# Optimization experiments

Measured on AMD Instinct MI355X. Metric: run time of the kernel, lower is better.

## Reference

```python
import math
import jax, jax.numpy as jnp
import numpy as np

B, H, W, C = 2, 32, 32, 64
K = 15
G = 4
GC = C // G
K2 = K * K
RED = C // 4
MAX_SIGMA = 0.5


def setup_inputs() -> dict:
    key = jax.random.key(0)
    ks = jax.random.split(key, 32)
    f32 = jnp.float32

    def rn(k, shape, std):
        return (jax.random.normal(k, shape) * std).astype(f32)

    lin = 1.0 / math.sqrt(C)
    inp = {
        'x': jax.random.normal(ks[0], (B, H, W, C), f32),
        'raw_sigma': jnp.asarray(math.log(math.exp(0.3) - 1.0), f32),
        'base_offset_scale': jnp.asarray(0.1, f32),
        # input/output projections (stored [in,out])
        'w_ip': rn(ks[1], (C, C), lin), 'b_ip': jnp.zeros((C,), f32),
        'w_op': rn(ks[2], (C, C), lin), 'b_op': jnp.zeros((C,), f32),
        # dw_conv: depthwise 3x3 (HWIO, I=1) then pointwise 1x1 ([in,out])
        'w_dw': rn(ks[3], (3, 3, 1, C), 1.0 / 3.0), 'b_dw': jnp.zeros((C,), f32),
        'w_pw': rn(ks[4], (C, C), lin), 'b_pw': jnp.zeros((C,), f32),
        # offset / mask heads (original zero-inits; small random to exercise path)
        'w_off': rn(ks[5], (C, G * K2 * 2), 0.01), 'b_off': rn(ks[6], (G * K2 * 2,), 0.01),
        'w_msk': rn(ks[7], (C, G * K2), 0.01), 'b_msk': rn(ks[8], (G * K2,), 0.01),
        # kernel MLP: 2 -> 32 -> 32 -> G*GC
        'w_k1': rn(ks[9], (2, 32), 0.5), 'b_k1': jnp.zeros((32,), f32),
        'w_k2': rn(ks[10], (32, 32), 1.0 / math.sqrt(32)), 'b_k2': jnp.zeros((32,), f32),
        'w_k3': rn(ks[11], (32, G * GC), 1.0 / math.sqrt(32)), 'b_k3': jnp.zeros((G * GC,), f32),
        # SE block
        'w_fc1': rn(ks[12], (C, RED), lin), 'b_fc1': jnp.zeros((RED,), f32),
        'w_fc2': rn(ks[13], (RED, C), 1.0 / math.sqrt(RED)), 'b_fc2': jnp.zeros((C,), f32),
    }
    return inp


def _forward(x, raw_sigma, base_offset_scale, w_ip, b_ip, w_op, b_op, w_dw, b_dw,
             w_pw, b_pw, w_off, b_off, w_msk, b_msk, w_k1, b_k1, w_k2, b_k2,
             w_k3, b_k3, w_fc1, b_fc1, w_fc2, b_fc2):
    Bx, Hx, Wx, Cx = x.shape
    sigma = jnp.clip(jax.nn.softplus(raw_sigma), 1e-3, MAX_SIGMA)
    grid = jnp.linspace(-0.5, 0.5, K)  # [K]

    x_proj = x @ w_ip + b_ip  # [B,H,W,C]

    # depthwise 3x3 (SAME) + SiLU + pointwise 1x1
    y = jax.lax.conv_general_dilated(
        x, w_dw, (1, 1), 'SAME',
        dimension_numbers=('NHWC', 'HWIO', 'NHWC'), feature_group_count=Cx) + b_dw
    x_dw = jax.nn.silu(y) @ w_pw + b_pw  # [B,H,W,C]

    # Gaussian envelope over kernel grid, normalized
    env = jnp.exp(-(grid[:, None] ** 2 + grid[None, :] ** 2) / (2.0 * sigma ** 2))
    env = env / jnp.maximum(env.sum(), 1e-8)
    env_flat = env.reshape(1, 1, 1, 1, K2)

    gh, gw = jnp.meshgrid(grid, grid, indexing='ij')
    pos = jnp.stack([gh.ravel(), gw.ravel()], axis=-1) * 2.0  # [K2,2]
    hkw = jax.nn.silu(pos @ w_k1 + b_k1)
    hkw = jax.nn.silu(hkw @ w_k2 + b_k2)
    kw_raw = hkw @ w_k3 + b_k3  # [K2, G*GC]
    # faithful to torch view quirk: (K,K,G,gc) memory reinterpreted as (G,K2,gc)
    kw = kw_raw.reshape(G, K2, GC).reshape(1, 1, 1, G, K2, GC)

    offsets = (x_dw @ w_off + b_off).reshape(Bx, Hx, Wx, G, K2, 2) * base_offset_scale
    raw_mask = (x_dw @ w_msk + b_msk).reshape(Bx, Hx, Wx, G, K2) * env_flat
    attn = jnp.nan_to_num(jax.nn.softmax(raw_mask, axis=-1))

    # absolute sampling locations
    ref = jnp.linspace(-(K // 2), K // 2, K)
    rh, rw = jnp.meshgrid(ref, ref, indexing='ij')  # [K,K]
    pos_h = jnp.arange(Hx, dtype=x.dtype).reshape(1, Hx, 1, 1, 1)
    pos_w = jnp.arange(Wx, dtype=x.dtype).reshape(1, 1, Wx, 1, 1)
    abs_h = pos_h + rh.ravel().reshape(1, 1, 1, 1, K2) + offsets[..., 0]
    abs_w = pos_w + rw.ravel().reshape(1, 1, 1, 1, K2) + offsets[..., 1]
    ah = jnp.clip(abs_h, 0.0, Hx - 1)
    aw = jnp.clip(abs_w, 0.0, Wx - 1)
    h_f = jnp.clip(jnp.floor(ah).astype(jnp.int32), 0, Hx - 1)
    w_f = jnp.clip(jnp.floor(aw).astype(jnp.int32), 0, Wx - 1)
    h_c = jnp.minimum(h_f + 1, Hx - 1)
    w_c = jnp.minimum(w_f + 1, Wx - 1)
    hw = ah - h_f.astype(x.dtype)
    ww = aw - w_f.astype(x.dtype)
    valid = (~((abs_h < 0) | (abs_h > Hx - 1) | (abs_w < 0) | (abs_w > Wx - 1))).astype(x.dtype)

    xg = x_proj.reshape(Bx, Hx, Wx, G, GC)
    b_idx = jnp.arange(Bx).reshape(Bx, 1, 1, 1, 1)
    g_idx = jnp.arange(G).reshape(1, 1, 1, G, 1)
    v_ff = xg[b_idx, h_f, w_f, g_idx]  # [B,H,W,G,K2,GC]
    v_fc = xg[b_idx, h_f, w_c, g_idx]
    v_cf = xg[b_idx, h_c, w_f, g_idx]
    v_cc = xg[b_idx, h_c, w_c, g_idx]
    sampled = (v_ff * ((1 - hw) * (1 - ww) * valid)[..., None]
               + v_fc * ((1 - hw) * ww * valid)[..., None]
               + v_cf * (hw * (1 - ww) * valid)[..., None]
               + v_cc * (hw * ww * valid)[..., None])
    sampled = sampled * kw
    output = (sampled * attn[..., None]).sum(axis=4).reshape(Bx, Hx, Wx, Cx)

    # SE block (no mask, no bias)
    pooled = output.mean(axis=(1, 2), keepdims=True)
    se = jax.nn.silu(pooled @ w_fc1 + b_fc1) @ w_fc2 + b_fc2
    output = output * jax.nn.sigmoid(se)

    out = output @ w_op + b_op
    offset_reg = (offsets ** 2).mean()
    entropy = -(attn * jnp.log(attn + 1e-8)).sum(axis=-1).mean()
    return out, offset_reg, -entropy


def reference(x, raw_sigma, base_offset_scale, w_ip, b_ip, w_op, b_op, w_dw, b_dw,
              w_pw, b_pw, w_off, b_off, w_msk, b_msk, w_k1, b_k1, w_k2, b_k2,
              w_k3, b_k3, w_fc1, b_fc1, w_fc2, b_fc2):
    return _forward(x, raw_sigma, base_offset_scale, w_ip, b_ip, w_op, b_op,
                    w_dw, b_dw, w_pw, b_pw, w_off, b_off, w_msk, b_msk,
                    w_k1, b_k1, w_k2, b_k2, w_k3, b_k3, w_fc1, b_fc1, w_fc2, b_fc2)
```

## Files before the change

### kernel.cpp

```cpp
#include <hip/hip_runtime.h>
#include <math.h>

#define KK2 225
#define NPIX 2048
#define OFFC 1800
#define MSKC 900

#define WS_KW    0
#define WS_XPROJ 16384
#define WS_XDW   (16384+131072)
#define WS_OUT   (16384+2*131072)
#define WS_POOL  (16384+3*131072)
#define WS_GATE  (WS_POOL+128)
#define WS_ENTP  (WS_GATE+128)
#define WS_OFFP  (WS_ENTP+2048)
#define WS_PART2 (WS_OFFP+512)

__device__ __forceinline__ float silu(float a) { return a / (1.f + __expf(-a)); }

__global__ __launch_bounds__(256) void k_pre(
    const float* __restrict__ x,
    const float* __restrict__ w_ip, const float* __restrict__ b_ip,
    const float* __restrict__ w_dw, const float* __restrict__ b_dw,
    const float* __restrict__ w_pw, const float* __restrict__ b_pw,
    const float* __restrict__ w_k1, const float* __restrict__ b_k1,
    const float* __restrict__ w_k2, const float* __restrict__ b_k2,
    const float* __restrict__ w_k3, const float* __restrict__ b_k3,
    float* __restrict__ ws)
{
  int t = threadIdx.x;
  if (blockIdx.x < 512) {
    int px = t >> 6, c = t & 63;
    int pix = blockIdx.x * 4 + px;
    int b = pix >> 10, h = (pix >> 5) & 31, w = pix & 31;
    __shared__ float xs[4][64], ys[4][64];
    xs[px][c] = x[pix*64 + c];
    float acc = b_dw[c];
    #pragma unroll
    for (int dh = -1; dh <= 1; dh++) {
      int hh = h + dh;
      if (hh < 0 || hh > 31) continue;
      #pragma unroll
      for (int dw2 = -1; dw2 <= 1; dw2++) {
        int wp = w + dw2;
        if (wp < 0 || wp > 31) continue;
        acc += x[(((b*32 + hh)*32 + wp) << 6) + c] * w_dw[((dh+1)*3 + (dw2+1))*64 + c];
      }
    }
    ys[px][c] = silu(acc);
    __syncthreads();
    float p1 = b_ip[c], p2 = b_pw[c];
    #pragma unroll 8
    for (int k = 0; k < 64; k++) {
      p1 += xs[px][k] * w_ip[k*64 + c];
      p2 += ys[px][k] * w_pw[k*64 + c];
    }
    ws[WS_XPROJ + pix*64 + c] = p1;
    ws[WS_XDW   + pix*64 + c] = p2;
  } else {
    __shared__ float h1s[4][32], h2s[4][32];
    int tl = t >> 6, lane = t & 63;
    int tap = (blockIdx.x - 512) * 4 + tl;
    int tapc = min(tap, KK2 - 1);
    int i = tapc / 15, j = tapc % 15;
    float gi = -0.5f + (float)i * (1.0f/14.0f);
    float gj = -0.5f + (float)j * (1.0f/14.0f);
    float p0 = gi * 2.f, p1 = gj * 2.f;
    if (lane < 32) {
      float a = p0 * w_k1[lane] + p1 * w_k1[32 + lane] + b_k1[lane];
      h1s[tl][lane] = silu(a);
    }
    __syncthreads();
    if (lane < 32) {
      float a = b_k2[lane];
      #pragma unroll
      for (int q = 0; q < 32; q++) a += h1s[tl][q] * w_k2[q*32 + lane];
      h2s[tl][lane] = silu(a);
    }
    __syncthreads();
    float a = b_k3[lane];
    #pragma unroll
    for (int q = 0; q < 32; q++) a += h2s[tl][q] * w_k3[q*64 + lane];
    if (tap < KK2) ws[WS_KW + tap*64 + lane] = a;
  }
}

__global__ __launch_bounds__(512, 4) void k_main(
    const float* __restrict__ raw_sigma,
    const float* __restrict__ base_scale,
    const float* __restrict__ w_off, const float* __restrict__ b_off,
    const float* __restrict__ w_msk, const float* __restrict__ b_msk,
    float* __restrict__ ws)
{
  __shared__ float xdT[256];
  __shared__ float env_s[KK2];
  __shared__ float off_s[4*OFFC];
  __shared__ float msk_s[4*MSKC];
  __shared__ float red_s[16];
  __shared__ float ent_sh[16];
  __shared__ float env_sum;

  int t = threadIdx.x;
  int pix0 = blockIdx.x * 4;
  int b = pix0 >> 10;

  float sp = log1pf(__expf(raw_sigma[0]));
  float sigma = fminf(fmaxf(sp, 1e-3f), 0.5f);
  float envv = 0.f;
  if (t < KK2) {
    int i = t / 15, j = t % 15;
    float gi = -0.5f + (float)i * (1.0f/14.0f);
    float gj = -0.5f + (float)j * (1.0f/14.0f);
    envv = __expf(-(gi*gi + gj*gj) / (2.f*sigma*sigma));
  }
  if (t < 256) {
    int px = t >> 6, k = t & 63;
    xdT[k*4 + px] = ws[WS_XDW + (pix0 + px)*64 + k];
  }
  {
    float v = envv;
    #pragma unroll
    for (int m = 32; m > 0; m >>= 1) v += __shfl_xor(v, m);
    if ((t & 63) == 0) red_s[t >> 6] = v;
    __syncthreads();
    if (t == 0) {
      float s = 0.f;
      #pragma unroll
      for (int q = 0; q < 8; q++) s += red_s[q];
      env_sum = fmaxf(s, 1e-8f);
    }
    __syncthreads();
    if (t < KK2) env_s[t] = envv / env_sum;
  }

  int o0 = t, o1 = t + 512, o2 = t + 1024, o3 = t + 1536;
  int q0 = t, q1 = t + 512;
  int o3c = min(o3, OFFC - 1);
  int q1c = min(q1, MSKC - 1);
  const float* p0 = w_off + o0;
  const float* p1 = w_off + o1;
  const float* p2 = w_off + o2;
  const float* p3 = w_off + o3c;
  const float* p4 = w_msk + q0;
  const float* p5 = w_msk + q1c;
  float4 a0 = make_float4(b_off[o0], b_off[o0], b_off[o0], b_off[o0]);
  float4 a1 = make_float4(b_off[o1], b_off[o1], b_off[o1], b_off[o1]);
  float4 a2 = make_float4(b_off[o2], b_off[o2], b_off[o2], b_off[o2]);
  float4 a3 = make_float4(b_off[o3c], b_off[o3c], b_off[o3c], b_off[o3c]);
  float4 a4 = make_float4(b_msk[q0], b_msk[q0], b_msk[q0], b_msk[q0]);
  float4 a5 = make_float4(b_msk[q1c], b_msk[q1c], b_msk[q1c], b_msk[q1c]);
  const float4* xv = (const float4*)xdT;
  #pragma unroll 2
  for (int k = 0; k < 64; k++) {
    float4 xk = xv[k];
    float w0 = *p0, w1 = *p1, w2 = *p2, w3 = *p3, w4 = *p4, w5 = *p5;
    a0.x += xk.x*w0; a0.y += xk.y*w0; a0.z += xk.z*w0; a0.w += xk.w*w0;
    a1.x += xk.x*w1; a1.y += xk.y*w1; a1.z += xk.z*w1; a1.w += xk.w*w1;
    a2.x += xk.x*w2; a2.y += xk.y*w2; a2.z += xk.z*w2; a2.w += xk.w*w2;
    a3.x += xk.x*w3; a3.y += xk.y*w3; a3.z += xk.z*w3; a3.w += xk.w*w3;
    a4.x += xk.x*w4; a4.y += xk.y*w4; a4.z += xk.z*w4; a4.w += xk.w*w4;
    a5.x += xk.x*w5; a5.y += xk.y*w5; a5.z += xk.z*w5; a5.w += xk.w*w5;
    p0 += OFFC; p1 += OFFC; p2 += OFFC; p3 += OFFC; p4 += MSKC; p5 += MSKC;
  }
  float scale = base_scale[0];
  float offreg = 0.f;
  {
    float v;
    v = a0.x*scale; off_s[0*OFFC + o0] = v; offreg += v*v;
    v = a0.y*scale; off_s[1*OFFC + o0] = v; offreg += v*v;
    v = a0.z*scale; off_s[2*OFFC + o0] = v; offreg += v*v;
    v = a0.w*scale; off_s[3*OFFC + o0] = v; offreg += v*v;
    v = a1.x*scale; off_s[0*OFFC + o1] = v; offreg += v*v;
    v = a1.y*scale; off_s[1*OFFC + o1] = v; offreg += v*v;
    v = a1.z*scale; off_s[2*OFFC + o1] = v; offreg += v*v;
    v = a1.w*scale; off_s[3*OFFC + o1] = v; offreg += v*v;
    v = a2.x*scale; off_s[0*OFFC + o2] = v; offreg += v*v;
    v = a2.y*scale; off_s[1*OFFC + o2] = v; offreg += v*v;
    v = a2.z*scale; off_s[2*OFFC + o2] = v; offreg += v*v;
    v = a2.w*scale; off_s[3*OFFC + o2] = v; offreg += v*v;
    if (o3 < OFFC) {
      v = a3.x*scale; off_s[0*OFFC + o3] = v; offreg += v*v;
      v = a3.y*scale; off_s[1*OFFC + o3] = v; offreg += v*v;
      v = a3.z*scale; off_s[2*OFFC + o3] = v; offreg += v*v;
      v = a3.w*scale; off_s[3*OFFC + o3] = v; offreg += v*v;
    }
    msk_s[0*MSKC + q0] = a4.x; msk_s[1*MSKC + q0] = a4.y;
    msk_s[2*MSKC + q0] = a4.z; msk_s[3*MSKC + q0] = a4.w;
    if (q1 < MSKC) {
      msk_s[0*MSKC + q1] = a5.x; msk_s[1*MSKC + q1] = a5.y;
      msk_s[2*MSKC + q1] = a5.z; msk_s[3*MSKC + q1] = a5.w;
    }
  }
  {
    #pragma unroll
    for (int m = 32; m > 0; m >>= 1) offreg += __shfl_xor(offreg, m);
    __syncthreads();
    if ((t & 63) == 0) red_s[t >> 6] = offreg;
    __syncthreads();
    if (t == 0) {
      float s = 0.f;
      #pragma unroll
      for (int q = 0; q < 8; q++) s += red_s[q];
      ws[WS_OFFP + blockIdx.x] = s;
    }
  }

  int wv = t >> 6, lane = t & 63;
  #pragma unroll
  for (int rep = 0; rep < 2; rep++) {
    int pair = wv + rep*8;
    int px = pair >> 2, g = pair & 3;
    float v[4];
    float m = -INFINITY;
    #pragma unroll
    for (int kk = 0; kk < 4; kk++) {
      int p = lane + kk*64;
      if (p < KK2) { v[kk] = msk_s[px*MSKC + g*KK2 + p] * env_s[p]; m = fmaxf(m, v[kk]); }
      else v[kk] = -INFINITY;
    }
    #pragma unroll
    for (int s = 32; s > 0; s >>= 1) m = fmaxf(m, __shfl_xor(m, s));
    float sum = 0.f;
    #pragma unroll
    for (int kk = 0; kk < 4; kk++) {
      int p = lane + kk*64;
      if (p < KK2) { v[kk] = __expf(v[kk] - m); sum += v[kk]; }
    }
    #pragma unroll
    for (int s = 32; s > 0; s >>= 1) sum += __shfl_xor(sum, s);
    float inv = 1.f / sum;
    float ent = 0.f;
    #pragma unroll
    for (int kk = 0; kk < 4; kk++) {
      int p = lane + kk*64;
      if (p < KK2) {
        float a = v[kk] * inv;
        msk_s[px*MSKC + g*KK2 + p] = a;
        ent += a * __logf(a + 1e-8f);
      }
    }
    #pragma unroll
    for (int s = 32; s > 0; s >>= 1) ent += __shfl_xor(ent, s);
    if (lane == 0) ent_sh[pair] = ent;
  }
  __syncthreads();
  if (t < 4) ws[WS_ENTP + pix0 + t] =
      ent_sh[t*4] + ent_sh[t*4+1] + ent_sh[t*4+2] + ent_sh[t*4+3];

  const float* xp = ws + WS_XPROJ + (size_t)(b << 10)*64;
  int ts = lane >> 2, cl = lane & 3;
  #pragma unroll
  for (int rep = 0; rep < 2; rep++) {
    int pair = wv + rep*8;
    int px = pair >> 2, g = pair & 3;
    int pix = pix0 + px;
    int h = (pix >> 5) & 31, w = pix & 31;
    int cb = g*16 + cl*4;
    float4 acc = make_float4(0.f, 0.f, 0.f, 0.f);
    for (int p = ts; p < KK2; p += 16) {
      float at = msk_s[px*MSKC + g*KK2 + p];
      float2 o01 = *(const float2*)&off_s[px*OFFC + g*450 + p*2];
      float abs_h = (float)(h + (p/15 - 7)) + o01.x;
      float abs_w = (float)(w + (p%15 - 7)) + o01.y;
      float ah = fminf(fmaxf(abs_h, 0.f), 31.f);
      float aw = fminf(fmaxf(abs_w, 0.f), 31.f);
      int hf = (int)floorf(ah);
      int wf = (int)floorf(aw);
      int hc = min(hf + 1, 31), wc = min(wf + 1, 31);
      float hw_ = ah - (float)hf, ww_ = aw - (float)wf;
      float s = (abs_h < 0.f || abs_h > 31.f || abs_w < 0.f || abs_w > 31.f) ? 0.f : at;
      float w00 = (1.f-hw_)*(1.f-ww_)*s, w01 = (1.f-hw_)*ww_*s;
      float w10 = hw_*(1.f-ww_)*s,       w11 = hw_*ww_*s;
      const float4 vff = *(const float4*)&xp[((hf*32 + wf) << 6) + cb];
      const float4 vfc = *(const float4*)&xp[((hf*32 + wc) << 6) + cb];
      const float4 vcf = *(const float4*)&xp[((hc*32 + wf) << 6) + cb];
      const float4 vcc = *(const float4*)&xp[((hc*32 + wc) << 6) + cb];
      const float4 kwv = *(const float4*)&ws[WS_KW + g*3600 + p*16 + cl*4];
      acc.x += (vff.x*w00 + vfc.x*w01 + vcf.x*w10 + vcc.x*w11) * kwv.x;
      acc.y += (vff.y*w00 + vfc.y*w01 + vcf.y*w10 + vcc.y*w11) * kwv.y;
      acc.z += (vff.z*w00 + vfc.z*w01 + vcf.z*w10 + vcc.z*w11) * kwv.z;
      acc.w += (vff.w*w00 + vfc.w*w01 + vcf.w*w10 + vcc.w*w11) * kwv.w;
    }
    #pragma unroll
    for (int m = 4; m < 64; m <<= 1) {
      acc.x += __shfl_xor(acc.x, m);
      acc.y += __shfl_xor(acc.y, m);
      acc.z += __shfl_xor(acc.z, m);
      acc.w += __shfl_xor(acc.w, m);
    }
    if (lane < 4) *(float4*)&ws[WS_OUT + pix*64 + cb] = acc;
  }
}

__global__ __launch_bounds__(256) void k_red(float* __restrict__ ws, float* __restrict__ d_out)
{
  __shared__ float red[256];
  int t = threadIdx.x, blk = blockIdx.x;
  if (blk < 64) {
    int b = blk >> 5, chunk = blk & 31;
    int c = t & 63, str = t >> 6;
    const float* base = ws + WS_OUT + (size_t)((b*1024 + chunk*32) << 6) + c;
    float s = 0.f;
    #pragma unroll
    for (int i = 0; i < 8; i++) s += base[((str + i*4) << 6)];
    red[t] = s;
    __syncthreads();
    if (t < 64) ws[WS_PART2 + blk*64 + t] =
      red[t] + red[t+64] + red[t+128] + red[t+192];
  } else if (blk == 64) {
    float s = 0.f;
    #pragma unroll
    for (int i = 0; i < 8; i++) s += ws[WS_ENTP + t + i*256];
    #pragma unroll
    for (int m = 32; m > 0; m >>= 1) s += __shfl_xor(s, m);
    if ((t & 63) == 0) red[t >> 6] = s;
    __syncthreads();
    if (t == 0) d_out[NPIX*64 + 1] = (red[0] + red[1] + red[2] + red[3]) * (1.f/8192.f);
  } else {
    float s = 0.f;
    #pragma unroll
    for (int i = 0; i < 2; i++) s += ws[WS_OFFP + t + i*256];
    #pragma unroll
    for (int m = 32; m > 0; m >>= 1) s += __shfl_xor(s, m);
    if ((t & 63) == 0) red[t >> 6] = s;
    __syncthreads();
    if (t == 0) d_out[NPIX*64] = (red[0] + red[1] + red[2] + red[3]) * (1.f/3686400.f);
  }
}

__global__ __launch_bounds__(128) void k_se(
    const float* __restrict__ w_fc1, const float* __restrict__ b_fc1,
    const float* __restrict__ w_fc2, const float* __restrict__ b_fc2,
    float* __restrict__ ws)
{
  __shared__ float pool_s[2][64];
  __shared__ float hsh[2][16];
  int t = threadIdx.x;
  int b = t >> 6, c = t & 63;
  {
    float s = 0.f;
    #pragma unroll
    for (int ch = 0; ch < 32; ch++) s += ws[WS_PART2 + (b*32 + ch)*64 + c];
    pool_s[b][c] = s * (1.f/1024.f);
  }
  __syncthreads();
  if (t < 32) {
    int bb = t >> 4, r = t & 15;
    float a = b_fc1[r];
    #pragma unroll 16
    for (int cc = 0; cc < 64; cc++) a += pool_s[bb][cc] * w_fc1[cc*16 + r];
    hsh[bb][r] = silu(a);
  }
  __syncthreads();
  float a = b_fc2[c];
  #pragma unroll
  for (int r = 0; r < 16; r++) a += hsh[b][r] * w_fc2[r*64 + c];
  ws[WS_GATE + b*64 + c] = 1.f / (1.f + __expf(-a));
}

__global__ __launch_bounds__(256) void k_final(
    const float* __restrict__ w_op, const float* __restrict__ b_op,
    const float* __restrict__ ws, float* __restrict__ d_out)
{
  int t = threadIdx.x;
  int px = t >> 6, c = t & 63;
  int pix = blockIdx.x * 4 + px;
  int b = pix >> 10;
  __shared__ float sc[4][64];
  sc[px][c] = ws[WS_OUT + pix*64 + c] * ws[WS_GATE + b*64 + c];
  __syncthreads();
  float a = b_op[c];
  #pragma unroll 8
  for (int k = 0; k < 64; k++) a += sc[px][k] * w_op[k*64 + c];
  d_out[pix*64 + c] = a;
}

extern "C" void kernel_launch(void* const* d_in, const int* in_sizes, int n_in,
                              void* d_out, int out_size, void* d_ws, size_t ws_size,
                              hipStream_t stream)
{
  const float* x     = (const float*)d_in[0];
  const float* rsig  = (const float*)d_in[1];
  const float* bos   = (const float*)d_in[2];
  const float* w_ip  = (const float*)d_in[3];
  const float* b_ip  = (const float*)d_in[4];
  const float* w_op  = (const float*)d_in[5];
  const float* b_op  = (const float*)d_in[6];
  const float* w_dw  = (const float*)d_in[7];
  const float* b_dw  = (const float*)d_in[8];
  const float* w_pw  = (const float*)d_in[9];
  const float* b_pw  = (const float*)d_in[10];
  const float* w_off = (const float*)d_in[11];
  const float* b_off = (const float*)d_in[12];
  const float* w_msk = (const float*)d_in[13];
  const float* b_msk = (const float*)d_in[14];
  const float* w_k1  = (const float*)d_in[15];
  const float* b_k1  = (const float*)d_in[16];
  const float* w_k2  = (const float*)d_in[17];
  const float* b_k2  = (const float*)d_in[18];
  const float* w_k3  = (const float*)d_in[19];
  const float* b_k3  = (const float*)d_in[20];
  const float* w_fc1 = (const float*)d_in[21];
  const float* b_fc1 = (const float*)d_in[22];
  const float* w_fc2 = (const float*)d_in[23];
  const float* b_fc2 = (const float*)d_in[24];
  float* ws  = (float*)d_ws;
  float* out = (float*)d_out;

  hipLaunchKernelGGL(k_pre, dim3(569), dim3(256), 0, stream,
                     x, w_ip, b_ip, w_dw, b_dw, w_pw, b_pw,
                     w_k1, b_k1, w_k2, b_k2, w_k3, b_k3, ws);
  hipLaunchKernelGGL(k_main, dim3(512), dim3(512), 0, stream,
                     rsig, bos, w_off, b_off, w_msk, b_msk, ws);
  hipLaunchKernelGGL(k_red, dim3(66), dim3(256), 0, stream, ws, out);
  hipLaunchKernelGGL(k_se, dim3(1), dim3(128), 0, stream,
                     w_fc1, b_fc1, w_fc2, b_fc2, ws);
  hipLaunchKernelGGL(k_final, dim3(512), dim3(256), 0, stream,
                     w_op, b_op, ws, out);
}
```

Baseline: 54.04 us.

## Use 1024-thread blocks in k_main to spread offset/mask GEMV and sampling

Doubles the k_main block size to 1024 threads so each thread computes three output columns of the offset/mask projection instead of six. Each of the 16 (pixel, group) pairs now gets its own wavefront for the softmax and sampling phases, replacing the two-iteration rep loops. The goal is more parallelism and lower per-thread serial work and register pressure per block. The cost is larger blocks with more expensive barriers, and the occupancy hint is dropped, which may limit how many blocks can co-reside per CU.

```diff
diff --git a/kernel.cpp b/kernel.cpp
--- a/kernel.cpp
+++ b/kernel.cpp
@@ -85,7 +85,7 @@
   }
 }
 
-__global__ __launch_bounds__(512, 4) void k_main(
+__global__ __launch_bounds__(1024) void k_main(
     const float* __restrict__ raw_sigma,
     const float* __restrict__ base_scale,
     const float* __restrict__ w_off, const float* __restrict__ b_off,
@@ -101,6 +101,7 @@
   __shared__ float env_sum;
 
   int t = threadIdx.x;
+  int wv = t >> 6, lane = t & 63;
   int pix0 = blockIdx.x * 4;
   int b = pix0 >> 10;
 
@@ -121,95 +122,80 @@
     float v = envv;
     #pragma unroll
     for (int m = 32; m > 0; m >>= 1) v += __shfl_xor(v, m);
-    if ((t & 63) == 0) red_s[t >> 6] = v;
+    if (lane == 0) red_s[wv] = v;
     __syncthreads();
     if (t == 0) {
       float s = 0.f;
       #pragma unroll
-      for (int q = 0; q < 8; q++) s += red_s[q];
+      for (int q = 0; q < 16; q++) s += red_s[q];
       env_sum = fmaxf(s, 1e-8f);
     }
     __syncthreads();
     if (t < KK2) env_s[t] = envv / env_sum;
   }
 
-  int o0 = t, o1 = t + 512, o2 = t + 1024, o3 = t + 1536;
-  int q0 = t, q1 = t + 512;
-  int o3c = min(o3, OFFC - 1);
-  int q1c = min(q1, MSKC - 1);
-  const float* p0 = w_off + o0;
-  const float* p1 = w_off + o1;
-  const float* p2 = w_off + o2;
-  const float* p3 = w_off + o3c;
-  const float* p4 = w_msk + q0;
-  const float* p5 = w_msk + q1c;
-  float4 a0 = make_float4(b_off[o0], b_off[o0], b_off[o0], b_off[o0]);
-  float4 a1 = make_float4(b_off[o1], b_off[o1], b_off[o1], b_off[o1]);
-  float4 a2 = make_float4(b_off[o2], b_off[o2], b_off[o2], b_off[o2]);
-  float4 a3 = make_float4(b_off[o3c], b_off[o3c], b_off[o3c], b_off[o3c]);
-  float4 a4 = make_float4(b_msk[q0], b_msk[q0], b_msk[q0], b_msk[q0]);
-  float4 a5 = make_float4(b_msk[q1c], b_msk[q1c], b_msk[q1c], b_msk[q1c]);
+  float b0 = b_off[t];
+  float b1 = (t < 776) ? b_off[t + 1024] : b_msk[t - 776];
+  int  q2 = min(t + 248, MSKC - 1);
+  float b2 = b_msk[q2];
+  const float* p0 = w_off + t;
+  const float* p1 = (t < 776) ? (w_off + 1024 + t) : (w_msk + (t - 776));
+  int s1 = (t < 776) ? OFFC : MSKC;
+  const float* p2 = w_msk + q2;
+  float4 A0 = make_float4(b0,b0,b0,b0);
+  float4 A1 = make_float4(b1,b1,b1,b1);
+  float4 A2 = make_float4(b2,b2,b2,b2);
   const float4* xv = (const float4*)xdT;
-  #pragma unroll 2
+  #pragma unroll 4
   for (int k = 0; k < 64; k++) {
     float4 xk = xv[k];
-    float w0 = *p0, w1 = *p1, w2 = *p2, w3 = *p3, w4 = *p4, w5 = *p5;
-    a0.x += xk.x*w0; a0.y += xk.y*w0; a0.z += xk.z*w0; a0.w += xk.w*w0;
-    a1.x += xk.x*w1; a1.y += xk.y*w1; a1.z += xk.z*w1; a1.w += xk.w*w1;
-    a2.x += xk.x*w2; a2.y += xk.y*w2; a2.z += xk.z*w2; a2.w += xk.w*w2;
-    a3.x += xk.x*w3; a3.y += xk.y*w3; a3.z += xk.z*w3; a3.w += xk.w*w3;
-    a4.x += xk.x*w4; a4.y += xk.y*w4; a4.z += xk.z*w4; a4.w += xk.w*w4;
-    a5.x += xk.x*w5; a5.y += xk.y*w5; a5.z += xk.z*w5; a5.w += xk.w*w5;
-    p0 += OFFC; p1 += OFFC; p2 += OFFC; p3 += OFFC; p4 += MSKC; p5 += MSKC;
+    float w0 = *p0, w1 = *p1, w2 = *p2;
+    A0.x += xk.x*w0; A0.y += xk.y*w0; A0.z += xk.z*w0; A0.w += xk.w*w0;
+    A1.x += xk.x*w1; A1.y += xk.y*w1; A1.z += xk.z*w1; A1.w += xk.w*w1;
+    A2.x += xk.x*w2; A2.y += xk.y*w2; A2.z += xk.z*w2; A2.w += xk.w*w2;
+    p0 += OFFC; p1 += s1; p2 += MSKC;
   }
   float scale = base_scale[0];
   float offreg = 0.f;
   {
     float v;
-    v = a0.x*scale; off_s[0*OFFC + o0] = v; offreg += v*v;
-    v = a0.y*scale; off_s[1*OFFC + o0] = v; offreg += v*v;
-    v = a0.z*scale; off_s[2*OFFC + o0] = v; offreg += v*v;
-    v = a0.w*scale; off_s[3*OFFC + o0] = v; offreg += v*v;
-    v = a1.x*scale; off_s[0*OFFC + o1] = v; offreg += v*v;
-    v = a1.y*scale; off_s[1*OFFC + o1] = v; offreg += v*v;
-    v = a1.z*scale; off_s[2*OFFC + o1] = v; offreg += v*v;
-    v = a1.w*scale; off_s[3*OFFC + o1] = v; offreg += v*v;
-    v = a2.x*scale; off_s[0*OFFC + o2] = v; offreg += v*v;
-    v = a2.y*scale; off_s[1*OFFC + o2] = v; offreg += v*v;
-    v = a2.z*scale; off_s[2*OFFC + o2] = v; offreg += v*v;
-    v = a2.w*scale; off_s[3*OFFC + o2] = v; offreg += v*v;
-    if (o3 < OFFC) {
-      v = a3.x*scale; off_s[0*OFFC + o3] = v; offreg += v*v;
-      v = a3.y*scale; off_s[1*OFFC + o3] = v; offreg += v*v;
-      v = a3.z*scale; off_s[2*OFFC + o3] = v; offreg += v*v;
-      v = a3.w*scale; off_s[3*OFFC + o3] = v; offreg += v*v;
-    }
-    msk_s[0*MSKC + q0] = a4.x; msk_s[1*MSKC + q0] = a4.y;
-    msk_s[2*MSKC + q0] = a4.z; msk_s[3*MSKC + q0] = a4.w;
-    if (q1 < MSKC) {
-      msk_s[0*MSKC + q1] = a5.x; msk_s[1*MSKC + q1] = a5.y;
-      msk_s[2*MSKC + q1] = a5.z; msk_s[3*MSKC + q1] = a5.w;
+    v = A0.x*scale; off_s[0*OFFC + t] = v; offreg += v*v;
+    v = A0.y*scale; off_s[1*OFFC + t] = v; offreg += v*v;
+    v = A0.z*scale; off_s[2*OFFC + t] = v; offreg += v*v;
+    v = A0.w*scale; off_s[3*OFFC + t] = v; offreg += v*v;
+    if (t < 776) {
+      int o = t + 1024;
+      v = A1.x*scale; off_s[0*OFFC + o] = v; offreg += v*v;
+      v = A1.y*scale; off_s[1*OFFC + o] = v; offreg += v*v;
+      v = A1.z*scale; off_s[2*OFFC + o] = v; offreg += v*v;
+      v = A1.w*scale; off_s[3*OFFC + o] = v; offreg += v*v;
+    } else {
+      int q = t - 776;
+      msk_s[0*MSKC + q] = A1.x; msk_s[1*MSKC + q] = A1.y;
+      msk_s[2*MSKC + q] = A1.z; msk_s[3*MSKC + q] = A1.w;
+    }
+    if (t < 652) {
+      int q = t + 248;
+      msk_s[0*MSKC + q] = A2.x; msk_s[1*MSKC + q] = A2.y;
+      msk_s[2*MSKC + q] = A2.z; msk_s[3*MSKC + q] = A2.w;
     }
   }
   {
     #pragma unroll
     for (int m = 32; m > 0; m >>= 1) offreg += __shfl_xor(offreg, m);
     __syncthreads();
-    if ((t & 63) == 0) red_s[t >> 6] = offreg;
+    if (lane == 0) red_s[wv] = offreg;
     __syncthreads();
     if (t == 0) {
       float s = 0.f;
       #pragma unroll
-      for (int q = 0; q < 8; q++) s += red_s[q];
+      for (int q = 0; q < 16; q++) s += red_s[q];
       ws[WS_OFFP + blockIdx.x] = s;
     }
   }
 
-  int wv = t >> 6, lane = t & 63;
-  #pragma unroll
-  for (int rep = 0; rep < 2; rep++) {
-    int pair = wv + rep*8;
-    int px = pair >> 2, g = pair & 3;
+  {
+    int px = wv >> 2, g = wv & 3;
     float v[4];
     float m = -INFINITY;
     #pragma unroll
@@ -241,7 +227,7 @@
     }
     #pragma unroll
     for (int s = 32; s > 0; s >>= 1) ent += __shfl_xor(ent, s);
-    if (lane == 0) ent_sh[pair] = ent;
+    if (lane == 0) ent_sh[wv] = ent;
   }
   __syncthreads();
   if (t < 4) ws[WS_ENTP + pix0 + t] =
@@ -249,10 +235,8 @@
 
   const float* xp = ws + WS_XPROJ + (size_t)(b << 10)*64;
   int ts = lane >> 2, cl = lane & 3;
-  #pragma unroll
-  for (int rep = 0; rep < 2; rep++) {
-    int pair = wv + rep*8;
-    int px = pair >> 2, g = pair & 3;
+  {
+    int px = wv >> 2, g = wv & 3;
     int pix = pix0 + px;
     int h = (pix >> 5) & 31, w = pix & 31;
     int cb = g*16 + cl*4;
@@ -410,7 +394,7 @@
   hipLaunchKernelGGL(k_pre, dim3(569), dim3(256), 0, stream,
                      x, w_ip, b_ip, w_dw, b_dw, w_pw, b_pw,
                      w_k1, b_k1, w_k2, b_k2, w_k3, b_k3, ws);
-  hipLaunchKernelGGL(k_main, dim3(512), dim3(512), 0, stream,
+  hipLaunchKernelGGL(k_main, dim3(512), dim3(1024), 0, stream,
                      rsig, bos, w_off, b_off, w_msk, b_msk, ws);
   hipLaunchKernelGGL(k_red, dim3(66), dim3(256), 0, stream, ws, out);
   hipLaunchKernelGGL(k_se, dim3(1), dim3(128), 0, stream,
```

After: 56.47 us. 1.04x slower.
